# Optimization experiments

Measured on AMD Instinct MI355X. Metric: run time of the kernel, lower is better.

Reference implementation:

```python
import jax, jax.numpy as jnp
import numpy as np

HEAD_DIM = 256
ROTARY_DIM = 128  # max(2, int(0.5*256) rounded down to even)
HALF_ROT = ROTARY_DIM // 2   # 64
HALF_HEAD = HEAD_DIM // 2    # 128
WAVELENGTH = 10000.0
ROPE_SCALING = 1.0
SOFT_CAP = 50.0
EPS = 1e-6
NQ = 8
NKV = 4
GROUPS = NQ // NKV
NEG_INF = -1e9


def rms_norm(x, scale):
    # keras-hub Gemma RMSNorm: fp32 compute, out = x * rsqrt(mean(x^2)+eps) * (1+scale)
    x32 = x.astype(jnp.float32)
    var = jnp.mean(jnp.square(x32), axis=-1, keepdims=True)
    y = x32 * jax.lax.rsqrt(var + EPS)
    return (y * (1.0 + scale.astype(jnp.float32))).astype(x.dtype)


def l2_norm(x):
    # Gemma4VNorm: pure L2 normalization over head_dim, no learned scale
    x32 = x.astype(jnp.float32)
    ss = jnp.sum(jnp.square(x32), axis=-1, keepdims=True)
    return (x32 * jax.lax.rsqrt(ss + EPS)).astype(x.dtype)


def apply_partial_rope(x):
    # x: [B, S, N, HEAD_DIM]. Partial proportional rotation: only the first
    # HALF_ROT elements of each HALF_HEAD half get rotated. RoPE inverse freqs
    # use denominator_dim = HEAD_DIM (not rotary_dim).
    S = x.shape[1]
    inv_freq = 1.0 / (WAVELENGTH ** (jnp.arange(0, ROTARY_DIM, 2, dtype=jnp.float32) / HEAD_DIM))  # [HALF_ROT]
    pos = jnp.arange(S, dtype=jnp.float32) / ROPE_SCALING
    freq = pos[:, None] * inv_freq[None, :]             # [S, HALF_ROT]
    cos = jnp.cos(freq)[None, :, None, :].astype(x.dtype)
    sin = jnp.sin(freq)[None, :, None, :].astype(x.dtype)
    x1 = x[..., :HALF_HEAD]
    x2 = x[..., HALF_HEAD:]
    x1r, x1n = x1[..., :HALF_ROT], x1[..., HALF_ROT:]
    x2r, x2n = x2[..., :HALF_ROT], x2[..., HALF_ROT:]
    # rotate-half form: [x1r, x2r]*cos + [-x2r, x1r]*sin
    y1r = x1r * cos - x2r * sin
    y2r = x2r * cos + x1r * sin
    return jnp.concatenate([y1r, x1n, y2r, x2n], axis=-1)


def setup_inputs() -> dict:
    key = jax.random.key(0)
    ks = jax.random.split(key, 6)
    B, S, D = 2, 2048, 2048
    x = jax.random.normal(ks[0], (B, S, D), jnp.float32)
    # causal mask [B, S, S]
    attention_mask = jnp.broadcast_to(jnp.tril(jnp.ones((S, S), bool))[None], (B, S, S))
    w_scale = 0.02
    Wq = jax.random.normal(ks[1], (NQ, D, HEAD_DIM), jnp.float32) * w_scale
    Wk = jax.random.normal(ks[2], (NKV, D, HEAD_DIM), jnp.float32) * w_scale
    Wv = jax.random.normal(ks[3], (NKV, D, HEAD_DIM), jnp.float32) * w_scale
    Wo = jax.random.normal(ks[4], (NQ, HEAD_DIM, D), jnp.float32) * w_scale
    q_scale = jnp.zeros((HEAD_DIM,), jnp.float32)
    k_scale = jnp.zeros((HEAD_DIM,), jnp.float32)
    return {"x": x, "attention_mask": attention_mask, "Wq": Wq, "Wk": Wk,
            "Wv": Wv, "Wo": Wo, "q_scale": q_scale, "k_scale": k_scale}


def reference(x, attention_mask, Wq, Wk, Wv, Wo, q_scale, k_scale):
    B, S, D = x.shape
    q = jnp.einsum('btd,ndh->btnh', x, Wq)
    q = apply_partial_rope(rms_norm(q, q_scale))
    k = jnp.einsum('bsd,kdh->bskh', x, Wk)
    k = apply_partial_rope(rms_norm(k, k_scale))
    v = l2_norm(jnp.einsum('bsd,kdh->bskh', x, Wv))
    # grouped-query attention, scaling = 1.0 (Gemma4 relies on QK norm)
    qg = q.reshape(B, S, NKV, GROUPS, HEAD_DIM)
    logits = jnp.einsum('btkgh,bskh->bkgts', qg, k)
    # logit soft cap
    logits = jnp.tanh(logits / SOFT_CAP) * SOFT_CAP
    mask = attention_mask[:, None, None, :, :]
    logits = jnp.where(mask, logits, NEG_INF)
    probs = jax.nn.softmax(logits.astype(jnp.float32), axis=-1).astype(logits.dtype)
    out = jnp.einsum('bkgts,bskh->btkgh', probs, v).reshape(B, S, NQ, HEAD_DIM)
    return jnp.einsum('btnh,nhd->btd', out, Wo)
```

## Files before the change

kernel.cpp:

```cpp
#include <hip/hip_runtime.h>

#define AS1 __attribute__((address_space(1)))
#define AS3 __attribute__((address_space(3)))

typedef __attribute__((ext_vector_type(8))) _Float16 f16x8;
typedef __attribute__((ext_vector_type(4))) _Float16 f16x4;
typedef __attribute__((ext_vector_type(4))) float f32x4;

#define MFMA_K16(a, b, c) __builtin_amdgcn_mfma_f32_16x16x16f16(a, b, c, 0, 0, 0)

__device__ __forceinline__ unsigned short f2h(float f) {
    union { _Float16 h; unsigned short u; } v; v.h = (_Float16)f; return v.u;
}

__device__ __forceinline__ void gload16(const void* g, void* l) {
    __builtin_amdgcn_global_load_lds((const AS1 unsigned int*)g, (AS3 unsigned int*)l, 16, 0, 0);
}

#define GBAR() __builtin_amdgcn_s_barrier()
#define VM4()  asm volatile("s_waitcnt vmcnt(4)" ::: "memory")
#define VM0()  asm volatile("s_waitcnt vmcnt(0)" ::: "memory")

__global__ __launch_bounds__(256) void k_cvt(const float* __restrict__ src,
                                             unsigned short* __restrict__ dst, int n4) {
    int i = blockIdx.x * 256 + threadIdx.x;
    if (i >= n4) return;
    float4 v = ((const float4*)src)[i];
    ushort4 o;
    o.x = f2h(v.x); o.y = f2h(v.y); o.z = f2h(v.z); o.w = f2h(v.w);
    ((ushort4*)dst)[i] = o;
}

__global__ __launch_bounds__(256) void k_transpose_cvt(const float* __restrict__ src,
                                                       unsigned short* __restrict__ dst,
                                                       int ld_src, int ld_dst,
                                                       long zs_src, long zs_dst) {
    __shared__ float tile[32][33];
    long sb = (long)blockIdx.z * zs_src;
    long db = (long)blockIdx.z * zs_dst;
    int c0 = blockIdx.x * 32, r0 = blockIdx.y * 32;
    int tx = threadIdx.x, ty = threadIdx.y;
#pragma unroll
    for (int i = 0; i < 4; i++)
        tile[ty + i * 8][tx] = src[sb + (long)(r0 + ty + i * 8) * ld_src + c0 + tx];
    __syncthreads();
#pragma unroll
    for (int i = 0; i < 4; i++)
        dst[db + (long)(c0 + ty + i * 8) * ld_dst + r0 + tx] = f2h(tile[tx][ty + i * 8]);
}

template<int BUF, int MIH>
__device__ __forceinline__ void rdA(const unsigned short* SA, int wm, int fr, int g,
                                    f16x8 (&af)[4][2]) {
#pragma unroll
    for (int m = 0; m < 4; m++)
#pragma unroll
        for (int kk = 0; kk < 2; kk++) {
            int pos = wm * 64 + m * 16 + fr;
            af[m][kk] = *(const f16x8*)(SA + BUF * 16384 + MIH * 8192 + pos * 64 +
                                        (((kk * 4 + g) ^ (fr & 7)) << 3));
        }
}

template<int BUF, int NIH>
__device__ __forceinline__ void rdB(const unsigned short* SB, int wn, int fr, int g,
                                    f16x8 (&bf)[2][2]) {
#pragma unroll
    for (int ni2 = 0; ni2 < 2; ni2++)
#pragma unroll
        for (int kk = 0; kk < 2; kk++) {
            int pos = wn * 32 + ni2 * 16 + fr;
            bf[ni2][kk] = *(const f16x8*)(SB + BUF * 16384 + NIH * 8192 + pos * 64 +
                                          (((kk * 4 + g) ^ (fr & 7)) << 3));
        }
}

template<int MIH, int NIH>
__device__ __forceinline__ void mm16(f16x8 (&af)[4][2], f16x8 (&bf)[2][2], f32x4 (&acc)[8][4]) {
    __builtin_amdgcn_s_setprio(1);
#pragma unroll
    for (int m = 0; m < 4; m++)
#pragma unroll
        for (int ni2 = 0; ni2 < 2; ni2++)
#pragma unroll
            for (int kk = 0; kk < 2; kk++)
                acc[MIH * 4 + m][NIH * 2 + ni2] = __builtin_amdgcn_mfma_f32_16x16x32_f16(
                    af[m][kk], bf[ni2][kk], acc[MIH * 4 + m][NIH * 2 + ni2], 0, 0, 0);
    __builtin_amdgcn_s_setprio(0);
}

__global__ __launch_bounds__(512, 1) void k_gemm256(const unsigned short* __restrict__ A,
                                                    const unsigned short* __restrict__ Bt,
                                                    float* __restrict__ C,
                                                    int M, int N, int K, int nbx) {
    __shared__ __align__(16) unsigned short sm[65536];
    unsigned short* SA = sm;
    unsigned short* SB = sm + 32768;

    int tid = threadIdx.x, lane = tid & 63, wid = tid >> 6;
    int g = lane >> 4, fr = lane & 15;
    int wm = wid >> 2, wn = wid & 3;

    int bid = blockIdx.x;
    int sid = (bid & 7) * ((int)gridDim.x >> 3) + (bid >> 3);
    int by = sid / nbx, bx = sid % nbx;
    int rowA0 = by * 256, colB0 = bx * 256;

    f32x4 acc[8][4];
#pragma unroll
    for (int mi = 0; mi < 8; mi++)
#pragma unroll
        for (int ni = 0; ni < 4; ni++) acc[mi][ni] = (f32x4){0.f, 0.f, 0.f, 0.f};

    auto stA = [&](int buf, int h, int kt) {
#pragma unroll
        for (int t = 0; t < 2; t++) {
            int i = t * 512 + tid;
            int pos = i >> 3;
            int grow = rowA0 + ((pos >> 6) << 7) + h * 64 + (pos & 63);
            int cg = (i & 7) ^ (pos & 7);
            gload16(A + (size_t)grow * K + kt * 64 + cg * 8,
                    SA + buf * 16384 + h * 8192 + pos * 64 + (i & 7) * 8);
        }
    };
    auto stB = [&](int buf, int h, int kt) {
#pragma unroll
        for (int t = 0; t < 2; t++) {
            int i = t * 512 + tid;
            int pos = i >> 3;
            int gcol = colB0 + ((pos >> 5) << 6) + h * 32 + (pos & 31);
            int cg = (i & 7) ^ (pos & 7);
            gload16(Bt + (size_t)gcol * K + kt * 64 + cg * 8,
                    SB + buf * 16384 + h * 8192 + pos * 64 + (i & 7) * 8);
        }
    };

    int nT = K >> 6;
    stA(0, 0, 0); stB(0, 0, 0); stA(0, 1, 0); stB(0, 1, 0);
    stA(1, 0, 1); stB(1, 0, 1);
    VM4();
    GBAR();

    f16x8 af[4][2], bf[2][2];
    int nIt = nT >> 1;
    for (int it = 0; it < nIt; it++) {
        int T = it * 2;
        bool s36 = (T + 2 < nT), s78 = (T + 3 < nT);
        rdA<0, 0>(SA, wm, fr, g, af); rdB<0, 0>(SB, wn, fr, g, bf);
        stA(1, 1, T + 1);
        GBAR(); mm16<0, 0>(af, bf, acc); GBAR();
        rdB<0, 1>(SB, wn, fr, g, bf);
        stB(1, 1, T + 1);
        GBAR(); mm16<0, 1>(af, bf, acc); GBAR();
        rdA<0, 1>(SA, wm, fr, g, af); rdB<0, 0>(SB, wn, fr, g, bf);
        if (s36) stA(0, 0, T + 2);
        GBAR(); mm16<1, 0>(af, bf, acc); GBAR();
        rdB<0, 1>(SB, wn, fr, g, bf);
        if (s36) { stB(0, 0, T + 2); VM4(); } else { VM0(); }
        GBAR(); mm16<1, 1>(af, bf, acc); GBAR();
        rdA<1, 0>(SA, wm, fr, g, af); rdB<1, 0>(SB, wn, fr, g, bf);
        if (s36) stA(0, 1, T + 2);
        GBAR(); mm16<0, 0>(af, bf, acc); GBAR();
        rdB<1, 1>(SB, wn, fr, g, bf);
        if (s36) stB(0, 1, T + 2);
        GBAR(); mm16<0, 1>(af, bf, acc); GBAR();
        rdA<1, 1>(SA, wm, fr, g, af); rdB<1, 0>(SB, wn, fr, g, bf);
        if (s78) stA(1, 0, T + 3);
        GBAR(); mm16<1, 0>(af, bf, acc); GBAR();
        rdB<1, 1>(SB, wn, fr, g, bf);
        if (s78) { stB(1, 0, T + 3); VM4(); } else { VM0(); }
        GBAR(); mm16<1, 1>(af, bf, acc); GBAR();
    }

#pragma unroll
    for (int mi = 0; mi < 8; mi++) {
        int row = rowA0 + wm * 128 + mi * 16 + g * 4;
#pragma unroll
        for (int ni = 0; ni < 4; ni++) {
            int col = colB0 + wn * 64 + ni * 16 + fr;
#pragma unroll
            for (int r = 0; r < 4; r++)
                C[(size_t)(row + r) * N + col] = acc[mi][ni][r];
        }
    }
}

__global__ __launch_bounds__(256) void k_gemm_f16(const unsigned short* __restrict__ A,
                                                  const unsigned short* __restrict__ Bt,
                                                  float* __restrict__ C,
                                                  int M, int N, int K) {
    __shared__ unsigned short As[128 * 64];
    __shared__ unsigned short Bs[128 * 64];
    int tid = threadIdx.x;
    int lane = tid & 63, wid = tid >> 6;
    int g = lane >> 4, fr = lane & 15;
    int rowA0 = blockIdx.y * 128;
    int colB0 = blockIdx.x * 128;

    f32x4 zero = {0.f, 0.f, 0.f, 0.f};
    f32x4 acc[4][4];
#pragma unroll
    for (int mi = 0; mi < 4; mi++)
#pragma unroll
        for (int ni = 0; ni < 4; ni++) acc[mi][ni] = zero;

    const unsigned short* ag[4];
    const unsigned short* bg[4];
#pragma unroll
    for (int j = 0; j < 4; j++) {
        int id = j * 256 + tid;
        int r = id >> 3;
        int c = (id & 7) ^ (r & 7);
        ag[j] = A + (size_t)(rowA0 + r) * K + c * 8;
        bg[j] = Bt + (size_t)(colB0 + r) * K + c * 8;
    }

    int nK = K >> 6;
    for (int kt = 0; kt < nK; kt++) {
#pragma unroll
        for (int j = 0; j < 4; j++) {
            int id = j * 256 + tid;
            gload16(ag[j], As + id * 8);
            gload16(bg[j], Bs + id * 8);
            ag[j] += 64; bg[j] += 64;
        }
        __syncthreads();
#pragma unroll
        for (int kk = 0; kk < 2; kk++) {
            f16x8 af[4], bfr[4];
#pragma unroll
            for (int mi = 0; mi < 4; mi++) {
                int r = (wid >> 1) * 64 + mi * 16 + fr;
                af[mi] = *(const f16x8*)(As + r * 64 + ((((kk << 2) + g) ^ (r & 7)) << 3));
            }
#pragma unroll
            for (int ni = 0; ni < 4; ni++) {
                int r = (wid & 1) * 64 + ni * 16 + fr;
                bfr[ni] = *(const f16x8*)(Bs + r * 64 + ((((kk << 2) + g) ^ (r & 7)) << 3));
            }
#pragma unroll
            for (int mi = 0; mi < 4; mi++)
#pragma unroll
                for (int ni = 0; ni < 4; ni++)
                    acc[mi][ni] = __builtin_amdgcn_mfma_f32_16x16x32_f16(af[mi], bfr[ni], acc[mi][ni], 0, 0, 0);
        }
        __syncthreads();
    }

#pragma unroll
    for (int mi = 0; mi < 4; mi++) {
        int row = rowA0 + (wid >> 1) * 64 + mi * 16 + g * 4;
#pragma unroll
        for (int ni = 0; ni < 4; ni++) {
            int col = colB0 + (wid & 1) * 64 + ni * 16 + fr;
#pragma unroll
            for (int r = 0; r < 4; r++)
                C[(size_t)(row + r) * N + col] = acc[mi][ni][r];
        }
    }
}

__global__ __launch_bounds__(256) void k_norm_rope(float* __restrict__ qkv,
                                                   const float* __restrict__ q_scale,
                                                   const float* __restrict__ k_scale,
                                                   unsigned short* __restrict__ Qh,
                                                   unsigned short* __restrict__ Kh) {
    __shared__ float Y[256];
    __shared__ float red[4];
    int blk = blockIdx.x;
    int bt = blk >> 4, slot = blk & 15;
    int b = bt >> 11, t = bt & 2047;
    int h = threadIdx.x;
    int lane = h & 63, wid = h >> 6;

    float x = qkv[(size_t)bt * 4096 + slot * 256 + h];
    float v = x * x;
#pragma unroll
    for (int m = 1; m < 64; m <<= 1) v += __shfl_xor(v, m);
    if (lane == 0) red[wid] = v;
    __syncthreads();
    float ss = red[0] + red[1] + red[2] + red[3];

    float y;
    if (slot < 12) {
        float fac = rsqrtf(ss * (1.0f / 256.0f) + 1e-6f);
        const float* sc = (slot < 8) ? q_scale : k_scale;
        y = x * fac * (1.0f + sc[h]);
    } else {
        float fac = rsqrtf(ss + 1e-6f);
        y = x * fac;
    }
    Y[h] = y;
    __syncthreads();

    if (slot < 12) {
        float out;
        int hm = h & 127;
        if (hm < 64) {
            float inv = exp2f(-(float)hm * 0.10381025296522993f);
            float fr = (float)t * inv;
            float s = sinf(fr), c = cosf(fr);
            float y1 = Y[hm], y2 = Y[128 + hm];
            out = (h < 128) ? (y1 * c - y2 * s) : (y2 * c + y1 * s);
        } else {
            out = y;
        }
        unsigned short hv = f2h(out);
        if (slot < 8)
            Qh[((size_t)(b * 8 + slot) * 2048 + t) * 256 + h] = hv;
        else
            Kh[((size_t)(b * 4 + (slot - 8)) * 2048 + t) * 256 + h] = hv;
    } else {
        qkv[(size_t)bt * 4096 + slot * 256 + h] = y;
    }
}

__global__ __launch_bounds__(512, 2) void k_attn(const unsigned short* __restrict__ Qhg,
                                                 const unsigned short* __restrict__ Khg,
                                                 const unsigned short* __restrict__ Vtg,
                                                 unsigned short* __restrict__ attn) {
    __shared__ __align__(16) char smem[132096];
    unsigned short* Ks = (unsigned short*)smem;
    unsigned short* Vs = (unsigned short*)(smem + 65536);
    float* ML = (float*)(smem + 131072);
    float* X = (float*)smem;

    int id = blockIdx.x;
    int bkv = id & 7;
    int npar = (id >> 3) & 1;
    int pair = id >> 4;
    int b = bkv >> 2, kv = bkv & 3;
    int n = kv * 2 + npar;
    int bn = b * 8 + n;

    int tid = threadIdx.x, lane = tid & 63, wid = tid >> 6;
    int g = lane >> 4, fr = lane & 15;
    int r2 = wid & 3, c2 = wid >> 2;
    int g4 = g * 4;

    const unsigned short* Kh = Khg + (size_t)bkv * 2048 * 256;
    const unsigned short* Vh = Vtg + (size_t)bkv * 256 * 2048;
    const unsigned short* Qb = Qhg + (size_t)bn * 2048 * 256;

    const unsigned short* kb[4];
    const unsigned short* vb[4];
    int sdst[4];
#pragma unroll
    for (int t2 = 0; t2 < 4; t2++) {
        int c_ = t2 * 512 + tid;
        int r = c_ >> 5, c = (c_ & 31) ^ (r & 7);
        kb[t2] = Kh + (size_t)r * 256 + c * 8;
        int d = c_ >> 3, cv = (c_ & 7) ^ (d & 7);
        vb[t2] = Vh + (size_t)d * 2048 + cv * 8;
        sdst[t2] = c_ * 8;
    }

    int krbase[2];
#pragma unroll
    for (int t16 = 0; t16 < 2; t16++) krbase[t16] = (c2 * 32 + t16 * 16 + fr) * 256;
    int s7 = fr & 7;
    int vslot[2];
#pragma unroll
    for (int t16 = 0; t16 < 2; t16++) vslot[t16] = (((c2 * 4 + t16 * 2 + (g >> 1)) ^ s7) << 3) + (g & 1) * 4;

    for (int half = 0; half < 2; half++) {
        int j = half ? 31 - pair : pair;
        int q0 = j * 64 + r2 * 16;

        const unsigned short* qrow = Qb + (size_t)(q0 + fr) * 256;
        f16x8 aq[8];
#pragma unroll
        for (int kk = 0; kk < 8; kk++) aq[kk] = *(const f16x8*)(qrow + kk * 32 + g * 8);

        f32x4 zero4 = {0.f, 0.f, 0.f, 0.f};
        f32x4 o[16];
#pragma unroll
        for (int i2 = 0; i2 < 16; i2++) o[i2] = zero4;
        float m_run = -1e30f;
        float l_run = 0.f;

        auto STAGE = [&](int bufi, int kt2) {
#pragma unroll
            for (int t2 = 0; t2 < 4; t2++) {
                gload16(kb[t2] + (size_t)kt2 * 16384, Ks + bufi * 16384 + sdst[t2]);
                gload16(vb[t2] + kt2 * 64, Vs + bufi * 16384 + sdst[t2]);
            }
        };

        STAGE(0, 0);
        __syncthreads();

        for (int kt = 0; kt <= j; kt++) {
            int cur = kt & 1;
            if (kt < j) STAGE(cur ^ 1, kt + 1);

            const unsigned short* KH = Ks + cur * 16384;
            const unsigned short* VC = Vs + cur * 16384;
            int k0 = kt * 64;

            f32x4 se[2] = {zero4, zero4}, so2[2] = {zero4, zero4};
            __builtin_amdgcn_s_setprio(1);
#pragma unroll
            for (int kk = 0; kk < 8; kk += 2) {
#pragma unroll
                for (int t16 = 0; t16 < 2; t16++) {
                    f16x8 bk0 = *(const f16x8*)(KH + krbase[t16] + ((((kk << 2) + g) ^ s7) << 3));
                    f16x8 bk1 = *(const f16x8*)(KH + krbase[t16] + (((((kk + 1) << 2) + g) ^ s7) << 3));
                    se[t16] = __builtin_amdgcn_mfma_f32_16x16x32_f16(bk0, aq[kk], se[t16], 0, 0, 0);
                    so2[t16] = __builtin_amdgcn_mfma_f32_16x16x32_f16(bk1, aq[kk + 1], so2[t16], 0, 0, 0);
                }
            }
            __builtin_amdgcn_s_setprio(0);

            int qg = q0 + fr;
            float pv[2][4];
            float ml = -1e30f;
#pragma unroll
            for (int t16 = 0; t16 < 2; t16++)
#pragma unroll
                for (int r = 0; r < 4; r++) {
                    float s = se[t16][r] + so2[t16][r];
                    float e = __expf(0.04f * s);
                    s = 50.f - 100.f * __builtin_amdgcn_rcpf(1.f + e);
                    int key = k0 + c2 * 32 + t16 * 16 + g4 + r;
                    if (key > qg) s = -1e9f;
                    pv[t16][r] = s;
                    ml = fmaxf(ml, s);
                }
            ml = fmaxf(ml, __shfl_xor(ml, 16));
            ml = fmaxf(ml, __shfl_xor(ml, 32));

            if (__any(ml > m_run + 8.f)) {
                float mnew = fmaxf(m_run, ml);
                float swl = __expf(m_run - mnew);
                m_run = mnew;
                l_run *= swl;
                float swr[4];
#pragma unroll
                for (int r = 0; r < 4; r++) swr[r] = __shfl(swl, g4 + r);
#pragma unroll
                for (int nt = 0; nt < 16; nt++)
#pragma unroll
                    for (int r = 0; r < 4; r++) o[nt][r] *= swr[r];
            }

            f16x4 pf[2];
#pragma unroll
            for (int t16 = 0; t16 < 2; t16++)
#pragma unroll
                for (int r = 0; r < 4; r++) {
                    float p = __expf(pv[t16][r] - m_run);
                    l_run += p;
                    pf[t16][r] = (_Float16)p;
                }

            __builtin_amdgcn_s_setprio(1);
#pragma unroll
            for (int nt = 0; nt < 16; nt++) {
                int dbase = (nt * 16 + fr) * 64;
                f16x4 bv0 = *(const f16x4*)(VC + dbase + vslot[0]);
                f16x4 bv1 = *(const f16x4*)(VC + dbase + vslot[1]);
                o[nt] = MFMA_K16(pf[0], bv0, o[nt]);
                o[nt] = MFMA_K16(pf[1], bv1, o[nt]);
            }
            __builtin_amdgcn_s_setprio(0);
            __syncthreads();
        }

        float l2 = l_run + __shfl_xor(l_run, 16);
        l2 += __shfl_xor(l2, 32);
        if (lane < 16) {
            float* mlw = ML + ((c2 * 4 + r2) * 16 + lane) * 2;
            mlw[0] = m_run; mlw[1] = l2;
        }
        __syncthreads();
        float wO[4], li[4];
#pragma unroll
        for (int r = 0; r < 4; r++) {
            int qq = g4 + r;
            const float* p0 = ML + (r2 * 16 + qq) * 2;
            const float* p1 = ML + ((4 + r2) * 16 + qq) * 2;
            float m0 = p0[0], l0 = p0[1], m1 = p1[0], l1 = p1[1];
            float ms = fmaxf(m0, m1);
            float w0 = __expf(m0 - ms), w1 = __expf(m1 - ms);
            li[r] = __builtin_amdgcn_rcpf(fmaxf(l0 * w0 + l1 * w1, 1e-30f));
            wO[r] = c2 ? w1 : w0;
        }
        float* Xl = X + (r2 * 64 + lane) * 68;
        if (c2 == 1) {
#pragma unroll
            for (int nt = 0; nt < 16; nt++)
#pragma unroll
                for (int r = 0; r < 4; r++) Xl[nt * 4 + r] = o[nt][r] * wO[r];
        }
        __syncthreads();
        if (c2 == 0) {
#pragma unroll
            for (int nt = 0; nt < 16; nt++)
#pragma unroll
                for (int r = 0; r < 4; r++) {
                    float val = (o[nt][r] * wO[r] + Xl[nt * 4 + r]) * li[r];
                    int qr = q0 + g4 + r;
                    attn[(size_t)(b * 2048 + qr) * 2048 + n * 256 + nt * 16 + fr] = f2h(val);
                }
        }
        __syncthreads();
    }
}

extern "C" void kernel_launch(void* const* d_in, const int* in_sizes, int n_in,
                              void* d_out, int out_size, void* d_ws, size_t ws_size,
                              hipStream_t stream) {
    const float* x       = (const float*)d_in[0];
    const float* Wq      = (const float*)d_in[2];
    const float* Wk      = (const float*)d_in[3];
    const float* Wv      = (const float*)d_in[4];
    const float* Wo      = (const float*)d_in[5];
    const float* q_scale = (const float*)d_in[6];
    const float* k_scale = (const float*)d_in[7];
    float* out = (float*)d_out;
    char* ws = (char*)d_ws;

    const size_t MB = 1024 * 1024;
    unsigned short* xh    = (unsigned short*)ws;
    unsigned short* Qh    = (unsigned short*)ws;
    unsigned short* WT    = (unsigned short*)(ws + 16 * MB);
    unsigned short* Kh    = (unsigned short*)(ws + 16 * MB);
    unsigned short* Vt    = (unsigned short*)(ws + 24 * MB);
    unsigned short* WoT   = (unsigned short*)(ws + 32 * MB);
    float*          qkv   = (float*)(ws + 40 * MB);
    unsigned short* attnb = (unsigned short*)(ws + 40 * MB);

    dim3 tb(32, 8);
    k_cvt<<<dim3(8192), dim3(256), 0, stream>>>(x, xh, 2097152);
    k_transpose_cvt<<<dim3(8, 64, 8), tb, 0, stream>>>(Wq, WT, 256, 2048, 524288L, 524288L);
    k_transpose_cvt<<<dim3(8, 64, 4), tb, 0, stream>>>(Wk, WT + (size_t)2048 * 2048, 256, 2048, 524288L, 524288L);
    k_transpose_cvt<<<dim3(8, 64, 4), tb, 0, stream>>>(Wv, WT + (size_t)3072 * 2048, 256, 2048, 524288L, 524288L);

    k_gemm256<<<dim3(256), dim3(512), 0, stream>>>(xh, WT, qkv, 4096, 4096, 2048, 16);
    k_norm_rope<<<dim3(65536), dim3(256), 0, stream>>>(qkv, q_scale, k_scale, Qh, Kh);
    for (int b = 0; b < 2; b++)
        k_transpose_cvt<<<dim3(8, 64, 4), tb, 0, stream>>>(qkv + (size_t)b * 2048 * 4096 + 3072,
                                                           Vt + (size_t)b * 4 * 256 * 2048,
                                                           4096, 2048, 256L, 524288L);
    k_attn<<<dim3(256), dim3(512), 0, stream>>>(Qh, Kh, Vt, attnb);

    k_transpose_cvt<<<dim3(64, 64, 1), tb, 0, stream>>>(Wo, WoT, 2048, 2048, 0L, 0L);
    k_gemm_f16<<<dim3(16, 32), dim3(256), 0, stream>>>(attnb, WoT, out, 4096, 2048, 2048);
}
```

Before: 274.9 us.

## Split attention blocks per query tile, single-buffer K/V, reuse gemm256 for output projection

The attention kernel no longer loops over two query tiles per block. It launches twice as many blocks, one causal-balanced tile each, and drops the K/V double buffer so LDS use falls and launch bounds allow four blocks per CU. This raises parallelism and occupancy, but it gives up the overlap of global loads with compute inside a block. The output projection now uses the larger 256-tile GEMM kernel, and the small f16 GEMM is removed.

```diff
diff --git a/kernel.cpp b/kernel.cpp
--- a/kernel.cpp
+++ b/kernel.cpp
@@ -185,81 +185,6 @@
     }
 }
 
-__global__ __launch_bounds__(256) void k_gemm_f16(const unsigned short* __restrict__ A,
-                                                  const unsigned short* __restrict__ Bt,
-                                                  float* __restrict__ C,
-                                                  int M, int N, int K) {
-    __shared__ unsigned short As[128 * 64];
-    __shared__ unsigned short Bs[128 * 64];
-    int tid = threadIdx.x;
-    int lane = tid & 63, wid = tid >> 6;
-    int g = lane >> 4, fr = lane & 15;
-    int rowA0 = blockIdx.y * 128;
-    int colB0 = blockIdx.x * 128;
-
-    f32x4 zero = {0.f, 0.f, 0.f, 0.f};
-    f32x4 acc[4][4];
-#pragma unroll
-    for (int mi = 0; mi < 4; mi++)
-#pragma unroll
-        for (int ni = 0; ni < 4; ni++) acc[mi][ni] = zero;
-
-    const unsigned short* ag[4];
-    const unsigned short* bg[4];
-#pragma unroll
-    for (int j = 0; j < 4; j++) {
-        int id = j * 256 + tid;
-        int r = id >> 3;
-        int c = (id & 7) ^ (r & 7);
-        ag[j] = A + (size_t)(rowA0 + r) * K + c * 8;
-        bg[j] = Bt + (size_t)(colB0 + r) * K + c * 8;
-    }
-
-    int nK = K >> 6;
-    for (int kt = 0; kt < nK; kt++) {
-#pragma unroll
-        for (int j = 0; j < 4; j++) {
-            int id = j * 256 + tid;
-            gload16(ag[j], As + id * 8);
-            gload16(bg[j], Bs + id * 8);
-            ag[j] += 64; bg[j] += 64;
-        }
-        __syncthreads();
-#pragma unroll
-        for (int kk = 0; kk < 2; kk++) {
-            f16x8 af[4], bfr[4];
-#pragma unroll
-            for (int mi = 0; mi < 4; mi++) {
-                int r = (wid >> 1) * 64 + mi * 16 + fr;
-                af[mi] = *(const f16x8*)(As + r * 64 + ((((kk << 2) + g) ^ (r & 7)) << 3));
-            }
-#pragma unroll
-            for (int ni = 0; ni < 4; ni++) {
-                int r = (wid & 1) * 64 + ni * 16 + fr;
-                bfr[ni] = *(const f16x8*)(Bs + r * 64 + ((((kk << 2) + g) ^ (r & 7)) << 3));
-            }
-#pragma unroll
-            for (int mi = 0; mi < 4; mi++)
-#pragma unroll
-                for (int ni = 0; ni < 4; ni++)
-                    acc[mi][ni] = __builtin_amdgcn_mfma_f32_16x16x32_f16(af[mi], bfr[ni], acc[mi][ni], 0, 0, 0);
-        }
-        __syncthreads();
-    }
-
-#pragma unroll
-    for (int mi = 0; mi < 4; mi++) {
-        int row = rowA0 + (wid >> 1) * 64 + mi * 16 + g * 4;
-#pragma unroll
-        for (int ni = 0; ni < 4; ni++) {
-            int col = colB0 + (wid & 1) * 64 + ni * 16 + fr;
-#pragma unroll
-            for (int r = 0; r < 4; r++)
-                C[(size_t)(row + r) * N + col] = acc[mi][ni][r];
-        }
-    }
-}
-
 __global__ __launch_bounds__(256) void k_norm_rope(float* __restrict__ qkv,
                                                    const float* __restrict__ q_scale,
                                                    const float* __restrict__ k_scale,
@@ -315,28 +240,31 @@
     }
 }
 
-__global__ __launch_bounds__(512, 2) void k_attn(const unsigned short* __restrict__ Qhg,
+__global__ __launch_bounds__(512, 4) void k_attn(const unsigned short* __restrict__ Qhg,
                                                  const unsigned short* __restrict__ Khg,
                                                  const unsigned short* __restrict__ Vtg,
                                                  unsigned short* __restrict__ attn) {
-    __shared__ __align__(16) char smem[132096];
+    __shared__ __align__(16) char smem[70656];
     unsigned short* Ks = (unsigned short*)smem;
-    unsigned short* Vs = (unsigned short*)(smem + 65536);
-    float* ML = (float*)(smem + 131072);
+    unsigned short* Vs = (unsigned short*)(smem + 32768);
     float* X = (float*)smem;
+    float* ML = (float*)(smem + 69632);
 
     int id = blockIdx.x;
     int bkv = id & 7;
     int npar = (id >> 3) & 1;
-    int pair = id >> 4;
+    int pair = (id >> 4) & 15;
+    int half = id >> 8;
     int b = bkv >> 2, kv = bkv & 3;
     int n = kv * 2 + npar;
     int bn = b * 8 + n;
+    int j = half ? 31 - pair : pair;
 
     int tid = threadIdx.x, lane = tid & 63, wid = tid >> 6;
     int g = lane >> 4, fr = lane & 15;
     int r2 = wid & 3, c2 = wid >> 2;
     int g4 = g * 4;
+    int q0 = j * 64 + r2 * 16;
 
     const unsigned short* Kh = Khg + (size_t)bkv * 2048 * 256;
     const unsigned short* Vh = Vtg + (size_t)bkv * 256 * 2048;
@@ -363,148 +291,133 @@
 #pragma unroll
     for (int t16 = 0; t16 < 2; t16++) vslot[t16] = (((c2 * 4 + t16 * 2 + (g >> 1)) ^ s7) << 3) + (g & 1) * 4;
 
-    for (int half = 0; half < 2; half++) {
-        int j = half ? 31 - pair : pair;
-        int q0 = j * 64 + r2 * 16;
-
-        const unsigned short* qrow = Qb + (size_t)(q0 + fr) * 256;
-        f16x8 aq[8];
-#pragma unroll
-        for (int kk = 0; kk < 8; kk++) aq[kk] = *(const f16x8*)(qrow + kk * 32 + g * 8);
-
-        f32x4 zero4 = {0.f, 0.f, 0.f, 0.f};
-        f32x4 o[16];
-#pragma unroll
-        for (int i2 = 0; i2 < 16; i2++) o[i2] = zero4;
-        float m_run = -1e30f;
-        float l_run = 0.f;
-
-        auto STAGE = [&](int bufi, int kt2) {
-#pragma unroll
-            for (int t2 = 0; t2 < 4; t2++) {
-                gload16(kb[t2] + (size_t)kt2 * 16384, Ks + bufi * 16384 + sdst[t2]);
-                gload16(vb[t2] + kt2 * 64, Vs + bufi * 16384 + sdst[t2]);
+    const unsigned short* qrow = Qb + (size_t)(q0 + fr) * 256;
+    f16x8 aq[8];
+#pragma unroll
+    for (int kk = 0; kk < 8; kk++) aq[kk] = *(const f16x8*)(qrow + kk * 32 + g * 8);
+
+    f32x4 zero4 = {0.f, 0.f, 0.f, 0.f};
+    f32x4 o[16];
+#pragma unroll
+    for (int i2 = 0; i2 < 16; i2++) o[i2] = zero4;
+    float m_run = -1e30f;
+    float l_run = 0.f;
+
+    for (int kt = 0; kt <= j; kt++) {
+#pragma unroll
+        for (int t2 = 0; t2 < 4; t2++) {
+            gload16(kb[t2] + (size_t)kt * 16384, Ks + sdst[t2]);
+            gload16(vb[t2] + kt * 64, Vs + sdst[t2]);
+        }
+        __syncthreads();
+
+        int k0 = kt * 64;
+
+        f32x4 se[2] = {zero4, zero4}, so2[2] = {zero4, zero4};
+        __builtin_amdgcn_s_setprio(1);
+#pragma unroll
+        for (int kk = 0; kk < 8; kk += 2) {
+#pragma unroll
+            for (int t16 = 0; t16 < 2; t16++) {
+                f16x8 bk0 = *(const f16x8*)(Ks + krbase[t16] + ((((kk << 2) + g) ^ s7) << 3));
+                f16x8 bk1 = *(const f16x8*)(Ks + krbase[t16] + (((((kk + 1) << 2) + g) ^ s7) << 3));
+                se[t16] = __builtin_amdgcn_mfma_f32_16x16x32_f16(bk0, aq[kk], se[t16], 0, 0, 0);
+                so2[t16] = __builtin_amdgcn_mfma_f32_16x16x32_f16(bk1, aq[kk + 1], so2[t16], 0, 0, 0);
             }
-        };
-
-        STAGE(0, 0);
+        }
+        __builtin_amdgcn_s_setprio(0);
+
+        int qg = q0 + fr;
+        float pv[2][4];
+        float ml = -1e30f;
+#pragma unroll
+        for (int t16 = 0; t16 < 2; t16++)
+#pragma unroll
+            for (int r = 0; r < 4; r++) {
+                float s = se[t16][r] + so2[t16][r];
+                float e = __expf(0.04f * s);
+                s = 50.f - 100.f * __builtin_amdgcn_rcpf(1.f + e);
+                int key = k0 + c2 * 32 + t16 * 16 + g4 + r;
+                if (key > qg) s = -1e9f;
+                pv[t16][r] = s;
+                ml = fmaxf(ml, s);
+            }
+        ml = fmaxf(ml, __shfl_xor(ml, 16));
+        ml = fmaxf(ml, __shfl_xor(ml, 32));
+
+        if (__any(ml > m_run + 8.f)) {
+            float mnew = fmaxf(m_run, ml);
+            float swl = __expf(m_run - mnew);
+            m_run = mnew;
+            l_run *= swl;
+            float swr[4];
+#pragma unroll
+            for (int r = 0; r < 4; r++) swr[r] = __shfl(swl, g4 + r);
+#pragma unroll
+            for (int nt = 0; nt < 16; nt++)
+#pragma unroll
+                for (int r = 0; r < 4; r++) o[nt][r] *= swr[r];
+        }
+
+        f16x4 pf[2];
+#pragma unroll
+        for (int t16 = 0; t16 < 2; t16++)
+#pragma unroll
+            for (int r = 0; r < 4; r++) {
+                float p = __expf(pv[t16][r] - m_run);
+                l_run += p;
+                pf[t16][r] = (_Float16)p;
+            }
+
+        __builtin_amdgcn_s_setprio(1);
+#pragma unroll
+        for (int nt = 0; nt < 16; nt++) {
+            int dbase = (nt * 16 + fr) * 64;
+            f16x4 bv0 = *(const f16x4*)(Vs + dbase + vslot[0]);
+            f16x4 bv1 = *(const f16x4*)(Vs + dbase + vslot[1]);
+            o[nt] = MFMA_K16(pf[0], bv0, o[nt]);
+            o[nt] = MFMA_K16(pf[1], bv1, o[nt]);
+        }
+        __builtin_amdgcn_s_setprio(0);
         __syncthreads();
-
-        for (int kt = 0; kt <= j; kt++) {
-            int cur = kt & 1;
-            if (kt < j) STAGE(cur ^ 1, kt + 1);
-
-            const unsigned short* KH = Ks + cur * 16384;
-            const unsigned short* VC = Vs + cur * 16384;
-            int k0 = kt * 64;
-
-            f32x4 se[2] = {zero4, zero4}, so2[2] = {zero4, zero4};
-            __builtin_amdgcn_s_setprio(1);
-#pragma unroll
-            for (int kk = 0; kk < 8; kk += 2) {
-#pragma unroll
-                for (int t16 = 0; t16 < 2; t16++) {
-                    f16x8 bk0 = *(const f16x8*)(KH + krbase[t16] + ((((kk << 2) + g) ^ s7) << 3));
-                    f16x8 bk1 = *(const f16x8*)(KH + krbase[t16] + (((((kk + 1) << 2) + g) ^ s7) << 3));
-                    se[t16] = __builtin_amdgcn_mfma_f32_16x16x32_f16(bk0, aq[kk], se[t16], 0, 0, 0);
-                    so2[t16] = __builtin_amdgcn_mfma_f32_16x16x32_f16(bk1, aq[kk + 1], so2[t16], 0, 0, 0);
-                }
+    }
+
+    float l2 = l_run + __shfl_xor(l_run, 16);
+    l2 += __shfl_xor(l2, 32);
+    if (lane < 16) {
+        float* mlw = ML + ((c2 * 4 + r2) * 16 + lane) * 2;
+        mlw[0] = m_run; mlw[1] = l2;
+    }
+    __syncthreads();
+    float wO[4], li[4];
+#pragma unroll
+    for (int r = 0; r < 4; r++) {
+        int qq = g4 + r;
+        const float* p0 = ML + (r2 * 16 + qq) * 2;
+        const float* p1 = ML + ((4 + r2) * 16 + qq) * 2;
+        float m0 = p0[0], l0 = p0[1], m1 = p1[0], l1 = p1[1];
+        float ms = fmaxf(m0, m1);
+        float w0 = __expf(m0 - ms), w1 = __expf(m1 - ms);
+        li[r] = __builtin_amdgcn_rcpf(fmaxf(l0 * w0 + l1 * w1, 1e-30f));
+        wO[r] = c2 ? w1 : w0;
+    }
+    float* Xl = X + (r2 * 64 + lane) * 68;
+    if (c2 == 1) {
+#pragma unroll
+        for (int nt = 0; nt < 16; nt++)
+#pragma unroll
+            for (int r = 0; r < 4; r++) Xl[nt * 4 + r] = o[nt][r] * wO[r];
+    }
+    __syncthreads();
+    if (c2 == 0) {
+#pragma unroll
+        for (int nt = 0; nt < 16; nt++)
+#pragma unroll
+            for (int r = 0; r < 4; r++) {
+                float val = (o[nt][r] * wO[r] + Xl[nt * 4 + r]) * li[r];
+                int qr = q0 + g4 + r;
+                attn[(size_t)(b * 2048 + qr) * 2048 + n * 256 + nt * 16 + fr] = f2h(val);
             }
-            __builtin_amdgcn_s_setprio(0);
-
-            int qg = q0 + fr;
-            float pv[2][4];
-            float ml = -1e30f;
-#pragma unroll
-            for (int t16 = 0; t16 < 2; t16++)
-#pragma unroll
-                for (int r = 0; r < 4; r++) {
-                    float s = se[t16][r] + so2[t16][r];
-                    float e = __expf(0.04f * s);
-                    s = 50.f - 100.f * __builtin_amdgcn_rcpf(1.f + e);
-                    int key = k0 + c2 * 32 + t16 * 16 + g4 + r;
-                    if (key > qg) s = -1e9f;
-                    pv[t16][r] = s;
-                    ml = fmaxf(ml, s);
-                }
-            ml = fmaxf(ml, __shfl_xor(ml, 16));
-            ml = fmaxf(ml, __shfl_xor(ml, 32));
-
-            if (__any(ml > m_run + 8.f)) {
-                float mnew = fmaxf(m_run, ml);
-                float swl = __expf(m_run - mnew);
-                m_run = mnew;
-                l_run *= swl;
-                float swr[4];
-#pragma unroll
-                for (int r = 0; r < 4; r++) swr[r] = __shfl(swl, g4 + r);
-#pragma unroll
-                for (int nt = 0; nt < 16; nt++)
-#pragma unroll
-                    for (int r = 0; r < 4; r++) o[nt][r] *= swr[r];
-            }
-
-            f16x4 pf[2];
-#pragma unroll
-            for (int t16 = 0; t16 < 2; t16++)
-#pragma unroll
-                for (int r = 0; r < 4; r++) {
-                    float p = __expf(pv[t16][r] - m_run);
-                    l_run += p;
-                    pf[t16][r] = (_Float16)p;
-                }
-
-            __builtin_amdgcn_s_setprio(1);
-#pragma unroll
-            for (int nt = 0; nt < 16; nt++) {
-                int dbase = (nt * 16 + fr) * 64;
-                f16x4 bv0 = *(const f16x4*)(VC + dbase + vslot[0]);
-                f16x4 bv1 = *(const f16x4*)(VC + dbase + vslot[1]);
-                o[nt] = MFMA_K16(pf[0], bv0, o[nt]);
-                o[nt] = MFMA_K16(pf[1], bv1, o[nt]);
-            }
-            __builtin_amdgcn_s_setprio(0);
-            __syncthreads();
-        }
-
-        float l2 = l_run + __shfl_xor(l_run, 16);
-        l2 += __shfl_xor(l2, 32);
-        if (lane < 16) {
-            float* mlw = ML + ((c2 * 4 + r2) * 16 + lane) * 2;
-            mlw[0] = m_run; mlw[1] = l2;
-        }
-        __syncthreads();
-        float wO[4], li[4];
-#pragma unroll
-        for (int r = 0; r < 4; r++) {
-            int qq = g4 + r;
-            const float* p0 = ML + (r2 * 16 + qq) * 2;
-            const float* p1 = ML + ((4 + r2) * 16 + qq) * 2;
-            float m0 = p0[0], l0 = p0[1], m1 = p1[0], l1 = p1[1];
-            float ms = fmaxf(m0, m1);
-            float w0 = __expf(m0 - ms), w1 = __expf(m1 - ms);
-            li[r] = __builtin_amdgcn_rcpf(fmaxf(l0 * w0 + l1 * w1, 1e-30f));
-            wO[r] = c2 ? w1 : w0;
-        }
-        float* Xl = X + (r2 * 64 + lane) * 68;
-        if (c2 == 1) {
-#pragma unroll
-            for (int nt = 0; nt < 16; nt++)
-#pragma unroll
-                for (int r = 0; r < 4; r++) Xl[nt * 4 + r] = o[nt][r] * wO[r];
-        }
-        __syncthreads();
-        if (c2 == 0) {
-#pragma unroll
-            for (int nt = 0; nt < 16; nt++)
-#pragma unroll
-                for (int r = 0; r < 4; r++) {
-                    float val = (o[nt][r] * wO[r] + Xl[nt * 4 + r]) * li[r];
-                    int qr = q0 + g4 + r;
-                    attn[(size_t)(b * 2048 + qr) * 2048 + n * 256 + nt * 16 + fr] = f2h(val);
-                }
-        }
-        __syncthreads();
     }
 }
 
@@ -543,8 +456,8 @@
         k_transpose_cvt<<<dim3(8, 64, 4), tb, 0, stream>>>(qkv + (size_t)b * 2048 * 4096 + 3072,
                                                            Vt + (size_t)b * 4 * 256 * 2048,
                                                            4096, 2048, 256L, 524288L);
-    k_attn<<<dim3(256), dim3(512), 0, stream>>>(Qh, Kh, Vt, attnb);
+    k_attn<<<dim3(512), dim3(512), 0, stream>>>(Qh, Kh, Vt, attnb);
 
     k_transpose_cvt<<<dim3(64, 64, 1), tb, 0, stream>>>(Wo, WoT, 2048, 2048, 0L, 0L);
-    k_gemm_f16<<<dim3(16, 32), dim3(256), 0, stream>>>(attnb, WoT, out, 4096, 2048, 2048);
-}
+    k_gemm256<<<dim3(128), dim3(512), 0, stream>>>(attnb, WoT, out, 4096, 2048, 2048, 8);
+}
```

Result: slower. 360.3 us (+31.1%).

## Fuse weight/input prep kernels and restructure attention to per-wave full-key tiles

Applied to the files above, without the earlier changes.

Merges the x conversion, the Q/K/V weight transposes and the Wo transpose into one k_prep launch, cutting the number of small kernel launches. The attention kernel now gives each block one 128-row query tile, with each of the 8 waves owning 16 rows across all 64 keys of every tile. This removes the split-key LDS merge and its extra barriers. In exchange it drops the balanced pairing of causal query tiles (j and 31-j), so block work now ranges from 2 to 32 key tiles, and per-tile work per wave doubles.

```diff
diff --git a/kernel.cpp b/kernel.cpp
--- a/kernel.cpp
+++ b/kernel.cpp
@@ -21,14 +21,51 @@
 #define VM4()  asm volatile("s_waitcnt vmcnt(4)" ::: "memory")
 #define VM0()  asm volatile("s_waitcnt vmcnt(0)" ::: "memory")
 
-__global__ __launch_bounds__(256) void k_cvt(const float* __restrict__ src,
-                                             unsigned short* __restrict__ dst, int n4) {
-    int i = blockIdx.x * 256 + threadIdx.x;
-    if (i >= n4) return;
-    float4 v = ((const float4*)src)[i];
-    ushort4 o;
-    o.x = f2h(v.x); o.y = f2h(v.y); o.z = f2h(v.z); o.w = f2h(v.w);
-    ((ushort4*)dst)[i] = o;
+__global__ __launch_bounds__(256) void k_prep(const float* __restrict__ x,
+                                              const float* __restrict__ Wq,
+                                              const float* __restrict__ Wk,
+                                              const float* __restrict__ Wv,
+                                              const float* __restrict__ Wo,
+                                              unsigned short* __restrict__ xh,
+                                              unsigned short* __restrict__ WT,
+                                              unsigned short* __restrict__ WoT) {
+    int z = blockIdx.z;
+    if (z == 24) {
+        int blk = blockIdx.y * 8 + blockIdx.x;
+        int t = threadIdx.y * 32 + threadIdx.x;
+        const float4* s4 = (const float4*)x;
+        ushort4* d4 = (ushort4*)xh;
+        int base = blk * 4096 + t;
+#pragma unroll
+        for (int i = 0; i < 16; i++) {
+            float4 v = s4[base + i * 256];
+            ushort4 u;
+            u.x = f2h(v.x); u.y = f2h(v.y); u.z = f2h(v.z); u.w = f2h(v.w);
+            d4[base + i * 256] = u;
+        }
+        return;
+    }
+    const float* src; unsigned short* dst;
+    int ld_src, c0, r0;
+    if (z < 16) {
+        if (z < 8)       { src = Wq + (size_t)z * 524288;        dst = WT + (size_t)z * 524288; }
+        else if (z < 12) { src = Wk + (size_t)(z - 8) * 524288;  dst = WT + (size_t)2048 * 2048 + (size_t)(z - 8) * 524288; }
+        else             { src = Wv + (size_t)(z - 12) * 524288; dst = WT + (size_t)3072 * 2048 + (size_t)(z - 12) * 524288; }
+        ld_src = 256;
+        c0 = blockIdx.x * 32; r0 = blockIdx.y * 32;
+    } else {
+        src = Wo; dst = WoT; ld_src = 2048;
+        c0 = ((z - 16) * 8 + blockIdx.x) * 32; r0 = blockIdx.y * 32;
+    }
+    __shared__ float tile[32][33];
+    int tx = threadIdx.x, ty = threadIdx.y;
+#pragma unroll
+    for (int i = 0; i < 4; i++)
+        tile[ty + i * 8][tx] = src[(size_t)(r0 + ty + i * 8) * ld_src + c0 + tx];
+    __syncthreads();
+#pragma unroll
+    for (int i = 0; i < 4; i++)
+        dst[(size_t)(c0 + ty + i * 8) * 2048 + r0 + tx] = f2h(tile[tx][ty + i * 8]);
 }
 
 __global__ __launch_bounds__(256) void k_transpose_cvt(const float* __restrict__ src,
@@ -319,24 +356,23 @@
                                                  const unsigned short* __restrict__ Khg,
                                                  const unsigned short* __restrict__ Vtg,
                                                  unsigned short* __restrict__ attn) {
-    __shared__ __align__(16) char smem[132096];
-    unsigned short* Ks = (unsigned short*)smem;
-    unsigned short* Vs = (unsigned short*)(smem + 65536);
-    float* ML = (float*)(smem + 131072);
-    float* X = (float*)smem;
+    __shared__ __align__(16) unsigned short KV[65536];
+    unsigned short* Ks = KV;
+    unsigned short* Vs = KV + 32768;
 
     int id = blockIdx.x;
     int bkv = id & 7;
     int npar = (id >> 3) & 1;
-    int pair = id >> 4;
+    int qt = id >> 4;
     int b = bkv >> 2, kv = bkv & 3;
     int n = kv * 2 + npar;
     int bn = b * 8 + n;
+    int nkt = 2 * qt + 2;
 
     int tid = threadIdx.x, lane = tid & 63, wid = tid >> 6;
     int g = lane >> 4, fr = lane & 15;
-    int r2 = wid & 3, c2 = wid >> 2;
-    int g4 = g * 4;
+    int g4 = g * 4, s7 = fr & 7;
+    int q0 = qt * 128 + wid * 16;
 
     const unsigned short* Kh = Khg + (size_t)bkv * 2048 * 256;
     const unsigned short* Vh = Vtg + (size_t)bkv * 256 * 2048;
@@ -344,7 +380,7 @@
 
     const unsigned short* kb[4];
     const unsigned short* vb[4];
-    int sdst[4];
+    int sd[4];
 #pragma unroll
     for (int t2 = 0; t2 < 4; t2++) {
         int c_ = t2 * 512 + tid;
@@ -352,160 +388,128 @@
         kb[t2] = Kh + (size_t)r * 256 + c * 8;
         int d = c_ >> 3, cv = (c_ & 7) ^ (d & 7);
         vb[t2] = Vh + (size_t)d * 2048 + cv * 8;
-        sdst[t2] = c_ * 8;
-    }
-
-    int krbase[2];
-#pragma unroll
-    for (int t16 = 0; t16 < 2; t16++) krbase[t16] = (c2 * 32 + t16 * 16 + fr) * 256;
-    int s7 = fr & 7;
-    int vslot[2];
-#pragma unroll
-    for (int t16 = 0; t16 < 2; t16++) vslot[t16] = (((c2 * 4 + t16 * 2 + (g >> 1)) ^ s7) << 3) + (g & 1) * 4;
-
-    for (int half = 0; half < 2; half++) {
-        int j = half ? 31 - pair : pair;
-        int q0 = j * 64 + r2 * 16;
-
-        const unsigned short* qrow = Qb + (size_t)(q0 + fr) * 256;
-        f16x8 aq[8];
-#pragma unroll
-        for (int kk = 0; kk < 8; kk++) aq[kk] = *(const f16x8*)(qrow + kk * 32 + g * 8);
-
-        f32x4 zero4 = {0.f, 0.f, 0.f, 0.f};
-        f32x4 o[16];
-#pragma unroll
-        for (int i2 = 0; i2 < 16; i2++) o[i2] = zero4;
-        float m_run = -1e30f;
-        float l_run = 0.f;
-
-        auto STAGE = [&](int bufi, int kt2) {
-#pragma unroll
-            for (int t2 = 0; t2 < 4; t2++) {
-                gload16(kb[t2] + (size_t)kt2 * 16384, Ks + bufi * 16384 + sdst[t2]);
-                gload16(vb[t2] + kt2 * 64, Vs + bufi * 16384 + sdst[t2]);
+        sd[t2] = c_ * 8;
+    }
+
+    int krb[4], vsl[4];
+#pragma unroll
+    for (int t16 = 0; t16 < 4; t16++) {
+        krb[t16] = (t16 * 16 + fr) * 256;
+        vsl[t16] = (((t16 * 2 + (g >> 1)) ^ s7) << 3) + (g & 1) * 4;
+    }
+
+    const unsigned short* qrow = Qb + (size_t)(q0 + fr) * 256;
+    f16x8 aq[8];
+#pragma unroll
+    for (int kk = 0; kk < 8; kk++) aq[kk] = *(const f16x8*)(qrow + kk * 32 + g * 8);
+
+    f32x4 zero4 = {0.f, 0.f, 0.f, 0.f};
+    f32x4 o[16];
+#pragma unroll
+    for (int i2 = 0; i2 < 16; i2++) o[i2] = zero4;
+    float m_run = -1e30f;
+    float l_run = 0.f;
+
+    auto STAGE = [&](int bufi, int kt2) {
+#pragma unroll
+        for (int t2 = 0; t2 < 4; t2++) {
+            gload16(kb[t2] + (size_t)kt2 * 16384, Ks + bufi * 16384 + sd[t2]);
+            gload16(vb[t2] + kt2 * 64, Vs + bufi * 16384 + sd[t2]);
+        }
+    };
+
+    STAGE(0, 0);
+    __syncthreads();
+
+    for (int kt = 0; kt < nkt; kt++) {
+        int cur = kt & 1;
+        if (kt + 1 < nkt) STAGE(cur ^ 1, kt + 1);
+
+        const unsigned short* KH = Ks + cur * 16384;
+        const unsigned short* VC = Vs + cur * 16384;
+        int k0 = kt * 64;
+
+        f32x4 se[4] = {zero4, zero4, zero4, zero4};
+        __builtin_amdgcn_s_setprio(1);
+#pragma unroll
+        for (int kk = 0; kk < 8; kk++) {
+#pragma unroll
+            for (int t16 = 0; t16 < 4; t16++) {
+                f16x8 bk = *(const f16x8*)(KH + krb[t16] + ((((kk << 2) + g) ^ s7) << 3));
+                se[t16] = __builtin_amdgcn_mfma_f32_16x16x32_f16(bk, aq[kk], se[t16], 0, 0, 0);
             }
-        };
-
-        STAGE(0, 0);
+        }
+        __builtin_amdgcn_s_setprio(0);
+
+        int qg = q0 + fr;
+        float p4[4][4];
+        float ml = -1e30f;
+#pragma unroll
+        for (int t16 = 0; t16 < 4; t16++)
+#pragma unroll
+            for (int r = 0; r < 4; r++) {
+                float s = se[t16][r];
+                float e = __expf(0.04f * s);
+                s = 50.f - 100.f * __builtin_amdgcn_rcpf(1.f + e);
+                int key = k0 + t16 * 16 + g4 + r;
+                if (key > qg) s = -1e9f;
+                p4[t16][r] = s;
+                ml = fmaxf(ml, s);
+            }
+        ml = fmaxf(ml, __shfl_xor(ml, 16));
+        ml = fmaxf(ml, __shfl_xor(ml, 32));
+
+        if (__any(ml > m_run + 8.f)) {
+            float mnew = fmaxf(m_run, ml);
+            float swl = __expf(m_run - mnew);
+            m_run = mnew;
+            l_run *= swl;
+            float swr[4];
+#pragma unroll
+            for (int r = 0; r < 4; r++) swr[r] = __shfl(swl, g4 + r);
+#pragma unroll
+            for (int nt = 0; nt < 16; nt++)
+#pragma unroll
+                for (int r = 0; r < 4; r++) o[nt][r] *= swr[r];
+        }
+
+        f16x4 pf[4];
+#pragma unroll
+        for (int t16 = 0; t16 < 4; t16++)
+#pragma unroll
+            for (int r = 0; r < 4; r++) {
+                float p = __expf(p4[t16][r] - m_run);
+                l_run += p;
+                pf[t16][r] = (_Float16)p;
+            }
+
+        __builtin_amdgcn_s_setprio(1);
+#pragma unroll
+        for (int nt = 0; nt < 16; nt++) {
+            int dbase = (nt * 16 + fr) * 64;
+#pragma unroll
+            for (int t16 = 0; t16 < 4; t16++) {
+                f16x4 bv = *(const f16x4*)(VC + dbase + vsl[t16]);
+                o[nt] = MFMA_K16(pf[t16], bv, o[nt]);
+            }
+        }
+        __builtin_amdgcn_s_setprio(0);
         __syncthreads();
-
-        for (int kt = 0; kt <= j; kt++) {
-            int cur = kt & 1;
-            if (kt < j) STAGE(cur ^ 1, kt + 1);
-
-            const unsigned short* KH = Ks + cur * 16384;
-            const unsigned short* VC = Vs + cur * 16384;
-            int k0 = kt * 64;
-
-            f32x4 se[2] = {zero4, zero4}, so2[2] = {zero4, zero4};
-            __builtin_amdgcn_s_setprio(1);
-#pragma unroll
-            for (int kk = 0; kk < 8; kk += 2) {
-#pragma unroll
-                for (int t16 = 0; t16 < 2; t16++) {
-                    f16x8 bk0 = *(const f16x8*)(KH + krbase[t16] + ((((kk << 2) + g) ^ s7) << 3));
-                    f16x8 bk1 = *(const f16x8*)(KH + krbase[t16] + (((((kk + 1) << 2) + g) ^ s7) << 3));
-                    se[t16] = __builtin_amdgcn_mfma_f32_16x16x32_f16(bk0, aq[kk], se[t16], 0, 0, 0);
-                    so2[t16] = __builtin_amdgcn_mfma_f32_16x16x32_f16(bk1, aq[kk + 1], so2[t16], 0, 0, 0);
-                }
-            }
-            __builtin_amdgcn_s_setprio(0);
-
-            int qg = q0 + fr;
-            float pv[2][4];
-            float ml = -1e30f;
-#pragma unroll
-            for (int t16 = 0; t16 < 2; t16++)
-#pragma unroll
-                for (int r = 0; r < 4; r++) {
-                    float s = se[t16][r] + so2[t16][r];
-                    float e = __expf(0.04f * s);
-                    s = 50.f - 100.f * __builtin_amdgcn_rcpf(1.f + e);
-                    int key = k0 + c2 * 32 + t16 * 16 + g4 + r;
-                    if (key > qg) s = -1e9f;
-                    pv[t16][r] = s;
-                    ml = fmaxf(ml, s);
-                }
-            ml = fmaxf(ml, __shfl_xor(ml, 16));
-            ml = fmaxf(ml, __shfl_xor(ml, 32));
-
-            if (__any(ml > m_run + 8.f)) {
-                float mnew = fmaxf(m_run, ml);
-                float swl = __expf(m_run - mnew);
-                m_run = mnew;
-                l_run *= swl;
-                float swr[4];
-#pragma unroll
-                for (int r = 0; r < 4; r++) swr[r] = __shfl(swl, g4 + r);
-#pragma unroll
-                for (int nt = 0; nt < 16; nt++)
-#pragma unroll
-                    for (int r = 0; r < 4; r++) o[nt][r] *= swr[r];
-            }
-
-            f16x4 pf[2];
-#pragma unroll
-            for (int t16 = 0; t16 < 2; t16++)
-#pragma unroll
-                for (int r = 0; r < 4; r++) {
-                    float p = __expf(pv[t16][r] - m_run);
-                    l_run += p;
-                    pf[t16][r] = (_Float16)p;
-                }
-
-            __builtin_amdgcn_s_setprio(1);
-#pragma unroll
-            for (int nt = 0; nt < 16; nt++) {
-                int dbase = (nt * 16 + fr) * 64;
-                f16x4 bv0 = *(const f16x4*)(VC + dbase + vslot[0]);
-                f16x4 bv1 = *(const f16x4*)(VC + dbase + vslot[1]);
-                o[nt] = MFMA_K16(pf[0], bv0, o[nt]);
-                o[nt] = MFMA_K16(pf[1], bv1, o[nt]);
-            }
-            __builtin_amdgcn_s_setprio(0);
-            __syncthreads();
-        }
-
-        float l2 = l_run + __shfl_xor(l_run, 16);
-        l2 += __shfl_xor(l2, 32);
-        if (lane < 16) {
-            float* mlw = ML + ((c2 * 4 + r2) * 16 + lane) * 2;
-            mlw[0] = m_run; mlw[1] = l2;
-        }
-        __syncthreads();
-        float wO[4], li[4];
+    }
+
+    float l2 = l_run + __shfl_xor(l_run, 16);
+    l2 += __shfl_xor(l2, 32);
+    float li = __builtin_amdgcn_rcpf(fmaxf(l2, 1e-30f));
+    float lrow[4];
+#pragma unroll
+    for (int r = 0; r < 4; r++) lrow[r] = __shfl(li, g4 + r);
+#pragma unroll
+    for (int nt = 0; nt < 16; nt++)
 #pragma unroll
         for (int r = 0; r < 4; r++) {
-            int qq = g4 + r;
-            const float* p0 = ML + (r2 * 16 + qq) * 2;
-            const float* p1 = ML + ((4 + r2) * 16 + qq) * 2;
-            float m0 = p0[0], l0 = p0[1], m1 = p1[0], l1 = p1[1];
-            float ms = fmaxf(m0, m1);
-            float w0 = __expf(m0 - ms), w1 = __expf(m1 - ms);
-            li[r] = __builtin_amdgcn_rcpf(fmaxf(l0 * w0 + l1 * w1, 1e-30f));
-            wO[r] = c2 ? w1 : w0;
-        }
-        float* Xl = X + (r2 * 64 + lane) * 68;
-        if (c2 == 1) {
-#pragma unroll
-            for (int nt = 0; nt < 16; nt++)
-#pragma unroll
-                for (int r = 0; r < 4; r++) Xl[nt * 4 + r] = o[nt][r] * wO[r];
-        }
-        __syncthreads();
-        if (c2 == 0) {
-#pragma unroll
-            for (int nt = 0; nt < 16; nt++)
-#pragma unroll
-                for (int r = 0; r < 4; r++) {
-                    float val = (o[nt][r] * wO[r] + Xl[nt * 4 + r]) * li[r];
-                    int qr = q0 + g4 + r;
-                    attn[(size_t)(b * 2048 + qr) * 2048 + n * 256 + nt * 16 + fr] = f2h(val);
-                }
-        }
-        __syncthreads();
-    }
+            int qr = q0 + g4 + r;
+            attn[(size_t)(b * 2048 + qr) * 2048 + n * 256 + nt * 16 + fr] = f2h(o[nt][r] * lrow[r]);
+        }
 }
 
 extern "C" void kernel_launch(void* const* d_in, const int* in_sizes, int n_in,
@@ -532,10 +536,7 @@
     unsigned short* attnb = (unsigned short*)(ws + 40 * MB);
 
     dim3 tb(32, 8);
-    k_cvt<<<dim3(8192), dim3(256), 0, stream>>>(x, xh, 2097152);
-    k_transpose_cvt<<<dim3(8, 64, 8), tb, 0, stream>>>(Wq, WT, 256, 2048, 524288L, 524288L);
-    k_transpose_cvt<<<dim3(8, 64, 4), tb, 0, stream>>>(Wk, WT + (size_t)2048 * 2048, 256, 2048, 524288L, 524288L);
-    k_transpose_cvt<<<dim3(8, 64, 4), tb, 0, stream>>>(Wv, WT + (size_t)3072 * 2048, 256, 2048, 524288L, 524288L);
+    k_prep<<<dim3(8, 64, 25), tb, 0, stream>>>(x, Wq, Wk, Wv, Wo, xh, WT, WoT);
 
     k_gemm256<<<dim3(256), dim3(512), 0, stream>>>(xh, WT, qkv, 4096, 4096, 2048, 16);
     k_norm_rope<<<dim3(65536), dim3(256), 0, stream>>>(qkv, q_scale, k_scale, Qh, Kh);
@@ -545,6 +546,5 @@
                                                            4096, 2048, 256L, 524288L);
     k_attn<<<dim3(256), dim3(512), 0, stream>>>(Qh, Kh, Vt, attnb);
 
-    k_transpose_cvt<<<dim3(64, 64, 1), tb, 0, stream>>>(Wo, WoT, 2048, 2048, 0L, 0L);
     k_gemm_f16<<<dim3(16, 32), dim3(256), 0, stream>>>(attnb, WoT, out, 4096, 2048, 2048);
 }
```

Result: slower. 309.4 us (+12.5%).
